# Kernel optimization log

Measured on AMD Instinct MI355X. Metric: run time of the kernel, lower is better.

## Reference

```python
import jax, jax.numpy as jnp
import numpy as np

H = 1024      # hidden_dim
V = 50257     # output_dim (vocab)
L = 512       # max_length


def setup_inputs() -> dict:
    key = jax.random.key(0)
    ks = jax.random.split(key, 12)
    s = 0.02
    return {
        "x": jax.random.randint(ks[0], (1,), 0, V),
        "hidden": jax.random.normal(ks[1], (1, 1, H), jnp.float32),
        "encoder_outputs": jax.random.normal(ks[2], (L, H), jnp.float32),
        "emb": jax.random.normal(ks[3], (V, H), jnp.float32) * s,
        "Ww": jax.random.normal(ks[4], (L, 2 * H), jnp.float32) * s,
        "bw": jnp.zeros((L,), jnp.float32),
        "Wc": jax.random.normal(ks[5], (H, 2 * H), jnp.float32) * s,
        "bc": jnp.zeros((H,), jnp.float32),
        "Wih": jax.random.normal(ks[6], (3 * H, H), jnp.float32) * s,
        "Whh": jax.random.normal(ks[7], (3 * H, H), jnp.float32) * s,
        "bih": jnp.zeros((3 * H,), jnp.float32),
        "bhh": jnp.zeros((3 * H,), jnp.float32),
        "Wo": jax.random.normal(ks[8], (V, H), jnp.float32) * s,
        "bo": jnp.zeros((V,), jnp.float32),
    }


def reference(x, hidden, encoder_outputs, emb, Ww, bw, Wc, bc, Wih, Whh, bih, bhh, Wo, bo):
    embed = emb[x].reshape(1, 1, -1)                      # [1,1,H]
    cat1 = jnp.concatenate([embed[0], hidden[0]], axis=1)  # [1,2H]
    weights = jax.nn.softmax(cat1 @ Ww.T + bw, axis=1)     # [1,L]
    wctx = weights @ encoder_outputs                       # [1,H]
    out = jnp.concatenate([embed[0], wctx], axis=1) @ Wc.T + bc  # [1,H]
    out = jax.nn.relu(out)
    # GRU cell (PyTorch gate layout: r, z, n)
    gi = out @ Wih.T + bih                                 # [1,3H]
    gh = hidden[0] @ Whh.T + bhh                           # [1,3H]
    r = jax.nn.sigmoid(gi[:, :H] + gh[:, :H])
    z = jax.nn.sigmoid(gi[:, H:2 * H] + gh[:, H:2 * H])
    n = jnp.tanh(gi[:, 2 * H:] + r * gh[:, 2 * H:])
    h_new = (1.0 - z) * n + z * hidden[0]                  # [1,H]
    logits = h_new @ Wo.T + bo                             # [1,V]
    out = jax.nn.log_softmax(logits, axis=1)
    return out, h_new[None], weights
```

## Files before the change

### kernel.cpp

```cpp
#include <hip/hip_runtime.h>
#include <math.h>

#define Hdim 1024
#define Vdim 50257
#define Ldim 512

__device__ __forceinline__ float waveReduceSum(float v) {
    #pragma unroll
    for (int off = 32; off > 0; off >>= 1) v += __shfl_down(v, off, 64);
    return v;
}
__device__ __forceinline__ float waveReduceMax(float v) {
    #pragma unroll
    for (int off = 32; off > 0; off >>= 1) v = fmaxf(v, __shfl_down(v, off, 64));
    return v;
}
template<int NW>
__device__ __forceinline__ float blockReduceSum(float v, float* red) {
    v = waveReduceSum(v);
    const int lane = threadIdx.x & 63, wid = threadIdx.x >> 6;
    if (lane == 0) red[wid] = v;
    __syncthreads();
    float s = red[0];
    #pragma unroll
    for (int i = 1; i < NW; i++) s += red[i];
    __syncthreads();
    return s;
}

__global__ __launch_bounds__(256) void k_att_gh(
    const int* __restrict__ xp, const float* __restrict__ hidden,
    const float* __restrict__ emb, const float* __restrict__ Ww,
    const float* __restrict__ bw, const float* __restrict__ Whh,
    const float* __restrict__ bhh, float* __restrict__ att, float* __restrict__ gh)
{
    __shared__ float red[4];
    const int t = threadIdx.x, bid = blockIdx.x;
    float acc = 0.f;
    if (bid < Ldim) {
        const int tok = xp[0];
        const float4* wrow = (const float4*)(Ww + (size_t)bid * (2 * Hdim));
        const float4* ev   = (const float4*)(emb + (size_t)tok * Hdim);
        const float4* hv   = (const float4*)hidden;
        #pragma unroll
        for (int k = 0; k < 2; ++k) {
            const int j = t * 2 + k;
            const float4 w = wrow[j];
            const float4 c = (j < Hdim / 4) ? ev[j] : hv[j - Hdim / 4];
            acc += w.x * c.x + w.y * c.y + w.z * c.z + w.w * c.w;
        }
        acc = blockReduceSum<4>(acc, red);
        if (t == 0) att[bid] = acc + bw[bid];
    } else {
        const int r = bid - Ldim;
        const float4* wrow = (const float4*)(Whh + (size_t)r * Hdim);
        const float4 w = wrow[t];
        const float4 h = ((const float4*)hidden)[t];
        acc = w.x * h.x + w.y * h.y + w.z * h.z + w.w * h.w;
        acc = blockReduceSum<4>(acc, red);
        if (t == 0) gh[r] = acc + bhh[r];
    }
}

__global__ __launch_bounds__(512) void k_softmax(
    const float* __restrict__ att, float* __restrict__ weights,
    float* __restrict__ out_w, float* __restrict__ wctx)
{
    __shared__ float red[8];
    __shared__ float bm, bs;
    const int t = threadIdx.x;
    const float v = att[t];
    float m = waveReduceMax(v);
    if ((t & 63) == 0) red[t >> 6] = m;
    __syncthreads();
    if (t == 0) {
        float mm = red[0];
        #pragma unroll
        for (int i = 1; i < 8; i++) mm = fmaxf(mm, red[i]);
        bm = mm;
    }
    __syncthreads();
    const float e = __expf(v - bm);
    float s = waveReduceSum(e);
    __syncthreads();
    if ((t & 63) == 0) red[t >> 6] = s;
    __syncthreads();
    if (t == 0) {
        float ss = red[0];
        #pragma unroll
        for (int i = 1; i < 8; i++) ss += red[i];
        bs = ss;
    }
    __syncthreads();
    const float w = e / bs;
    weights[t] = w;
    out_w[t]   = w;
    wctx[t] = 0.f; wctx[t + 512] = 0.f;
}

__global__ __launch_bounds__(256) void k_wctx(
    const float* __restrict__ weights, const float* __restrict__ enc,
    float* __restrict__ wctx)
{
    const int b = blockIdx.x, t = threadIdx.x;
    float4 acc = make_float4(0.f, 0.f, 0.f, 0.f);
    #pragma unroll
    for (int i = 0; i < 8; ++i) {
        const int l = b * 8 + i;
        const float w = weights[l];
        const float4 e = ((const float4*)(enc + (size_t)l * Hdim))[t];
        acc.x += w * e.x; acc.y += w * e.y; acc.z += w * e.z; acc.w += w * e.w;
    }
    atomicAdd(&wctx[t * 4 + 0], acc.x);
    atomicAdd(&wctx[t * 4 + 1], acc.y);
    atomicAdd(&wctx[t * 4 + 2], acc.z);
    atomicAdd(&wctx[t * 4 + 3], acc.w);
}

__global__ __launch_bounds__(256) void k_wc(
    const int* __restrict__ xp, const float* __restrict__ emb,
    const float* __restrict__ wctx, const float* __restrict__ Wc,
    const float* __restrict__ bc, float* __restrict__ cvec)
{
    __shared__ float red[4];
    const int t = threadIdx.x, r = blockIdx.x;
    const int tok = xp[0];
    const float4* wrow = (const float4*)(Wc + (size_t)r * (2 * Hdim));
    const float4* ev   = (const float4*)(emb + (size_t)tok * Hdim);
    const float4* cv   = (const float4*)wctx;
    float acc = 0.f;
    #pragma unroll
    for (int k = 0; k < 2; ++k) {
        const int j = t * 2 + k;
        const float4 w = wrow[j];
        const float4 c = (j < Hdim / 4) ? ev[j] : cv[j - Hdim / 4];
        acc += w.x * c.x + w.y * c.y + w.z * c.z + w.w * c.w;
    }
    acc = blockReduceSum<4>(acc, red);
    if (t == 0) cvec[r] = fmaxf(acc + bc[r], 0.f);
}

__global__ __launch_bounds__(256) void k_gru(
    const float* __restrict__ Wih, const float* __restrict__ bih,
    const float* __restrict__ gh, const float* __restrict__ cvec,
    const float* __restrict__ hidden, float* __restrict__ hnew,
    float* __restrict__ out_h)
{
    __shared__ float red[4];
    const int t = threadIdx.x, j = blockIdx.x;
    const float4 c = ((const float4*)cvec)[t];
    const float4 a = ((const float4*)(Wih + (size_t)j * Hdim))[t];
    const float4 b = ((const float4*)(Wih + (size_t)(j + Hdim) * Hdim))[t];
    const float4 d = ((const float4*)(Wih + (size_t)(j + 2 * Hdim) * Hdim))[t];
    float s0 = a.x * c.x + a.y * c.y + a.z * c.z + a.w * c.w;
    float s1 = b.x * c.x + b.y * c.y + b.z * c.z + b.w * c.w;
    float s2 = d.x * c.x + d.y * c.y + d.z * c.z + d.w * c.w;
    s0 = blockReduceSum<4>(s0, red);
    s1 = blockReduceSum<4>(s1, red);
    s2 = blockReduceSum<4>(s2, red);
    if (t == 0) {
        const float gir = s0 + bih[j];
        const float giz = s1 + bih[j + Hdim];
        const float gin = s2 + bih[j + 2 * Hdim];
        const float rr = 1.f / (1.f + __expf(-(gir + gh[j])));
        const float zz = 1.f / (1.f + __expf(-(giz + gh[j + Hdim])));
        const float nn = tanhf(gin + rr * gh[j + 2 * Hdim]);
        const float h = (1.f - zz) * nn + zz * hidden[j];
        hnew[j]  = h;
        out_h[j] = h;
    }
}

__global__ __launch_bounds__(256) void k_logits(
    const float* __restrict__ Wo, const float* __restrict__ bo,
    const float* __restrict__ h, float* __restrict__ logits)
{
    __shared__ float red[4];
    const int r = blockIdx.x, t = threadIdx.x;
    const float4 w = ((const float4*)(Wo + (size_t)r * Hdim))[t];
    const float4 hv = ((const float4*)h)[t];
    float acc = w.x * hv.x + w.y * hv.y + w.z * hv.z + w.w * hv.w;
    acc = waveReduceSum(acc);
    if ((t & 63) == 0) red[t >> 6] = acc;
    __syncthreads();
    if (t == 0) logits[r] = red[0] + red[1] + red[2] + red[3] + bo[r];
}

__global__ __launch_bounds__(256) void k_lse_part(
    const float* __restrict__ logits, float* __restrict__ pm, float* __restrict__ ps)
{
    __shared__ float redm[4], reds[4];
    const int gid = blockIdx.x * 256 + threadIdx.x;
    float m = -1e30f, s = 0.f;
    for (int i = gid; i < Vdim; i += 64 * 256) {
        const float v = logits[i];
        const float nm = fmaxf(m, v);
        s = s * __expf(m - nm) + __expf(v - nm);
        m = nm;
    }
    #pragma unroll
    for (int off = 32; off > 0; off >>= 1) {
        const float om = __shfl_down(m, off, 64);
        const float os = __shfl_down(s, off, 64);
        const float nm = fmaxf(m, om);
        s = s * __expf(m - nm) + os * __expf(om - nm);
        m = nm;
    }
    const int lane = threadIdx.x & 63, wid = threadIdx.x >> 6;
    if (lane == 0) { redm[wid] = m; reds[wid] = s; }
    __syncthreads();
    if (threadIdx.x == 0) {
        float M = redm[0], S = reds[0];
        #pragma unroll
        for (int i = 1; i < 4; i++) {
            const float nm = fmaxf(M, redm[i]);
            S = S * __expf(M - nm) + reds[i] * __expf(redm[i] - nm);
            M = nm;
        }
        pm[blockIdx.x] = M; ps[blockIdx.x] = S;
    }
}

__global__ __launch_bounds__(64) void k_lse_final(
    const float* __restrict__ pm, const float* __restrict__ ps,
    float* __restrict__ logZ)
{
    const int t = threadIdx.x;
    float m = pm[t], s = ps[t];
    #pragma unroll
    for (int off = 32; off > 0; off >>= 1) {
        const float om = __shfl_down(m, off, 64);
        const float os = __shfl_down(s, off, 64);
        const float nm = fmaxf(m, om);
        s = s * __expf(m - nm) + os * __expf(om - nm);
        m = nm;
    }
    if (t == 0) logZ[0] = m + logf(s);
}

__global__ __launch_bounds__(256) void k_out(
    float* __restrict__ out, const float* __restrict__ logZ)
{
    const int i = blockIdx.x * 256 + threadIdx.x;
    if (i < Vdim) out[i] = out[i] - logZ[0];
}

extern "C" void kernel_launch(void* const* d_in, const int* in_sizes, int n_in,
                              void* d_out, int out_size, void* d_ws, size_t ws_size,
                              hipStream_t stream)
{
    const int*   x      = (const int*)  d_in[0];
    const float* hidden = (const float*)d_in[1];
    const float* enc    = (const float*)d_in[2];
    const float* emb    = (const float*)d_in[3];
    const float* Ww     = (const float*)d_in[4];
    const float* bw     = (const float*)d_in[5];
    const float* Wc     = (const float*)d_in[6];
    const float* bc     = (const float*)d_in[7];
    const float* Wih    = (const float*)d_in[8];
    const float* Whh    = (const float*)d_in[9];
    const float* bih    = (const float*)d_in[10];
    const float* bhh    = (const float*)d_in[11];
    const float* Wo     = (const float*)d_in[12];
    const float* bo     = (const float*)d_in[13];

    float* out      = (float*)d_out;
    float* out_logp = out;
    float* out_h    = out + Vdim;
    float* out_w    = out + Vdim + Hdim;

    float* ws      = (float*)d_ws;
    float* att     = ws;
    float* weights = ws + 512;
    float* wctx    = ws + 1024;
    float* cvec    = ws + 2048;
    float* gh      = ws + 3072;
    float* hnew    = ws + 6144;
    float* pm      = ws + 7168;
    float* psum    = ws + 7232;
    float* logZ    = ws + 7296;

    k_att_gh   <<<dim3(Ldim + 3 * Hdim), dim3(256), 0, stream>>>(x, hidden, emb, Ww, bw, Whh, bhh, att, gh);
    k_softmax  <<<dim3(1),               dim3(512), 0, stream>>>(att, weights, out_w, wctx);
    k_wctx     <<<dim3(64),              dim3(256), 0, stream>>>(weights, enc, wctx);
    k_wc       <<<dim3(Hdim),            dim3(256), 0, stream>>>(x, emb, wctx, Wc, bc, cvec);
    k_gru      <<<dim3(Hdim),            dim3(256), 0, stream>>>(Wih, bih, gh, cvec, hidden, hnew, out_h);
    k_logits   <<<dim3(Vdim),            dim3(256), 0, stream>>>(Wo, bo, hnew, out_logp);
    k_lse_part <<<dim3(64),              dim3(256), 0, stream>>>(out_logp, pm, psum);
    k_lse_final<<<dim3(1),               dim3(64),  0, stream>>>(pm, psum, logZ);
    k_out      <<<dim3((Vdim + 255) / 256), dim3(256), 0, stream>>>(out_logp, logZ);
}
```

Measured before the change: 417.3 us.

## Fuse all decoder stages into one cooperative persistent kernel with grid syncs

Nine separate kernel launches become a single cooperative kernel of 256 blocks with 1024 threads each, using grid.sync between dependent phases. Each block redundantly computes the attention softmax into shared memory, replacing the separate softmax kernel and the atomic-based context accumulation. The logits GEMV now keeps one wave per row and folds the online log-sum-exp into the same pass, which removes the separate partial-reduction kernels. The aim is to cut launch overhead and extra passes over the logits. In exchange, each phase runs on a fixed 256-block grid with grid-wide barriers, and the 200MB Wo stream is read by fewer waves than before, which may lower memory-level parallelism.

```diff
diff --git a/kernel.cpp b/kernel.cpp
--- a/kernel.cpp
+++ b/kernel.cpp
@@ -1,9 +1,15 @@
 #include <hip/hip_runtime.h>
+#include <hip/hip_cooperative_groups.h>
 #include <math.h>
+
+namespace cg = cooperative_groups;
 
 #define Hdim 1024
 #define Vdim 50257
 #define Ldim 512
+#define NBLK 256
+#define NTHR 1024
+#define NWAVE 16
 
 __device__ __forceinline__ float waveReduceSum(float v) {
     #pragma unroll
@@ -15,234 +21,235 @@
     for (int off = 32; off > 0; off >>= 1) v = fmaxf(v, __shfl_down(v, off, 64));
     return v;
 }
-template<int NW>
-__device__ __forceinline__ float blockReduceSum(float v, float* red) {
-    v = waveReduceSum(v);
-    const int lane = threadIdx.x & 63, wid = threadIdx.x >> 6;
-    if (lane == 0) red[wid] = v;
-    __syncthreads();
-    float s = red[0];
-    #pragma unroll
-    for (int i = 1; i < NW; i++) s += red[i];
-    __syncthreads();
-    return s;
-}
-
-__global__ __launch_bounds__(256) void k_att_gh(
+__device__ __forceinline__ float dot4(float4 a, float4 b) {
+    return a.x * b.x + a.y * b.y + a.z * b.z + a.w * b.w;
+}
+
+__global__ __launch_bounds__(NTHR, 4) void k_fused(
     const int* __restrict__ xp, const float* __restrict__ hidden,
-    const float* __restrict__ emb, const float* __restrict__ Ww,
-    const float* __restrict__ bw, const float* __restrict__ Whh,
-    const float* __restrict__ bhh, float* __restrict__ att, float* __restrict__ gh)
+    const float* __restrict__ enc, const float* __restrict__ emb,
+    const float* __restrict__ Ww, const float* __restrict__ bw,
+    const float* __restrict__ Wc, const float* __restrict__ bc,
+    const float* __restrict__ Wih, const float* __restrict__ Whh,
+    const float* __restrict__ bih, const float* __restrict__ bhh,
+    const float* __restrict__ Wo, const float* __restrict__ bo,
+    float* __restrict__ out_logp, float* __restrict__ out_h,
+    float* __restrict__ out_w, float* __restrict__ ws)
 {
-    __shared__ float red[4];
-    const int t = threadIdx.x, bid = blockIdx.x;
-    float acc = 0.f;
-    if (bid < Ldim) {
-        const int tok = xp[0];
-        const float4* wrow = (const float4*)(Ww + (size_t)bid * (2 * Hdim));
-        const float4* ev   = (const float4*)(emb + (size_t)tok * Hdim);
-        const float4* hv   = (const float4*)hidden;
-        #pragma unroll
-        for (int k = 0; k < 2; ++k) {
-            const int j = t * 2 + k;
+    cg::grid_group grid = cg::this_grid();
+
+    __shared__ float sweights[Ldim];
+    __shared__ float red[NWAVE];
+    __shared__ float red2[NWAVE];
+    __shared__ float4 red4[8];
+    __shared__ float slz;
+
+    float* att  = ws;
+    float* gh   = ws + 512;
+    float* wctx = ws + 3584;
+    float* cvec = ws + 4608;
+    float* hnew = ws + 5632;
+    float* pm   = ws + 6656;
+    float* ps   = ws + 6912;
+
+    const int t = threadIdx.x, b = blockIdx.x;
+    const int lane = t & 63, iw = t >> 6;
+    const int tok = xp[0];
+    const float4* embv = (const float4*)(emb + (size_t)tok * Hdim);
+    const float4* hv   = (const float4*)hidden;
+
+    if (iw < 14) {
+        const int r = b * 14 + iw;
+        if (r < Ldim) {
+            const float4* wrow = (const float4*)(Ww + (size_t)r * (2 * Hdim));
+            float acc = 0.f;
+            #pragma unroll
+            for (int k = 0; k < 8; ++k) {
+                const int j = lane + 64 * k;
+                const float4 w = wrow[j];
+                const float4 c = (j < 256) ? embv[j] : hv[j - 256];
+                acc += dot4(w, c);
+            }
+            acc = waveReduceSum(acc);
+            if (lane == 0) att[r] = acc + bw[r];
+        } else {
+            const int r2 = r - Ldim;
+            const float4* wrow = (const float4*)(Whh + (size_t)r2 * Hdim);
+            float acc = 0.f;
+            #pragma unroll
+            for (int k = 0; k < 4; ++k) {
+                const int j = lane + 64 * k;
+                acc += dot4(wrow[j], hv[j]);
+            }
+            acc = waveReduceSum(acc);
+            if (lane == 0) gh[r2] = acc + bhh[r2];
+        }
+    }
+    grid.sync();
+
+    {
+        const float v = (t < Ldim) ? att[t] : -1e30f;
+        float wm = waveReduceMax(v);
+        if (lane == 0) red[iw] = wm;
+        __syncthreads();
+        float m = red[0];
+        #pragma unroll
+        for (int i = 1; i < NWAVE; ++i) m = fmaxf(m, red[i]);
+        const float e = (t < Ldim) ? __expf(v - m) : 0.f;
+        float wsum = waveReduceSum(e);
+        if (lane == 0) red2[iw] = wsum;
+        __syncthreads();
+        float s = red2[0];
+        #pragma unroll
+        for (int i = 1; i < NWAVE; ++i) s += red2[i];
+        if (t < Ldim) {
+            const float wgt = e / s;
+            sweights[t] = wgt;
+            if (b == 0) out_w[t] = wgt;
+        }
+    }
+
+    {
+        float4 acc = make_float4(0.f, 0.f, 0.f, 0.f);
+        if (t < Ldim) {
+            const float wgt = sweights[t];
+            const float4 e = *(const float4*)(enc + (size_t)t * Hdim + 4 * b);
+            acc.x = wgt * e.x; acc.y = wgt * e.y; acc.z = wgt * e.z; acc.w = wgt * e.w;
+        }
+        acc.x = waveReduceSum(acc.x);
+        acc.y = waveReduceSum(acc.y);
+        acc.z = waveReduceSum(acc.z);
+        acc.w = waveReduceSum(acc.w);
+        __syncthreads();
+        if (lane == 0 && iw < 8) red4[iw] = acc;
+        __syncthreads();
+        if (t == 0) {
+            float4 tot = red4[0];
+            #pragma unroll
+            for (int i = 1; i < 8; ++i) {
+                tot.x += red4[i].x; tot.y += red4[i].y;
+                tot.z += red4[i].z; tot.w += red4[i].w;
+            }
+            ((float4*)wctx)[b] = tot;
+        }
+    }
+    grid.sync();
+
+    if (iw < 4) {
+        const int r = b * 4 + iw;
+        const float4* wrow  = (const float4*)(Wc + (size_t)r * (2 * Hdim));
+        const float4* wctxv = (const float4*)wctx;
+        float acc = 0.f;
+        #pragma unroll
+        for (int k = 0; k < 8; ++k) {
+            const int j = lane + 64 * k;
             const float4 w = wrow[j];
-            const float4 c = (j < Hdim / 4) ? ev[j] : hv[j - Hdim / 4];
-            acc += w.x * c.x + w.y * c.y + w.z * c.z + w.w * c.w;
-        }
-        acc = blockReduceSum<4>(acc, red);
-        if (t == 0) att[bid] = acc + bw[bid];
-    } else {
-        const int r = bid - Ldim;
-        const float4* wrow = (const float4*)(Whh + (size_t)r * Hdim);
-        const float4 w = wrow[t];
-        const float4 h = ((const float4*)hidden)[t];
-        acc = w.x * h.x + w.y * h.y + w.z * h.z + w.w * h.w;
-        acc = blockReduceSum<4>(acc, red);
-        if (t == 0) gh[r] = acc + bhh[r];
-    }
-}
-
-__global__ __launch_bounds__(512) void k_softmax(
-    const float* __restrict__ att, float* __restrict__ weights,
-    float* __restrict__ out_w, float* __restrict__ wctx)
-{
-    __shared__ float red[8];
-    __shared__ float bm, bs;
-    const int t = threadIdx.x;
-    const float v = att[t];
-    float m = waveReduceMax(v);
-    if ((t & 63) == 0) red[t >> 6] = m;
-    __syncthreads();
-    if (t == 0) {
-        float mm = red[0];
-        #pragma unroll
-        for (int i = 1; i < 8; i++) mm = fmaxf(mm, red[i]);
-        bm = mm;
-    }
-    __syncthreads();
-    const float e = __expf(v - bm);
-    float s = waveReduceSum(e);
-    __syncthreads();
-    if ((t & 63) == 0) red[t >> 6] = s;
-    __syncthreads();
-    if (t == 0) {
-        float ss = red[0];
-        #pragma unroll
-        for (int i = 1; i < 8; i++) ss += red[i];
-        bs = ss;
-    }
-    __syncthreads();
-    const float w = e / bs;
-    weights[t] = w;
-    out_w[t]   = w;
-    wctx[t] = 0.f; wctx[t + 512] = 0.f;
-}
-
-__global__ __launch_bounds__(256) void k_wctx(
-    const float* __restrict__ weights, const float* __restrict__ enc,
-    float* __restrict__ wctx)
-{
-    const int b = blockIdx.x, t = threadIdx.x;
-    float4 acc = make_float4(0.f, 0.f, 0.f, 0.f);
-    #pragma unroll
-    for (int i = 0; i < 8; ++i) {
-        const int l = b * 8 + i;
-        const float w = weights[l];
-        const float4 e = ((const float4*)(enc + (size_t)l * Hdim))[t];
-        acc.x += w * e.x; acc.y += w * e.y; acc.z += w * e.z; acc.w += w * e.w;
-    }
-    atomicAdd(&wctx[t * 4 + 0], acc.x);
-    atomicAdd(&wctx[t * 4 + 1], acc.y);
-    atomicAdd(&wctx[t * 4 + 2], acc.z);
-    atomicAdd(&wctx[t * 4 + 3], acc.w);
-}
-
-__global__ __launch_bounds__(256) void k_wc(
-    const int* __restrict__ xp, const float* __restrict__ emb,
-    const float* __restrict__ wctx, const float* __restrict__ Wc,
-    const float* __restrict__ bc, float* __restrict__ cvec)
-{
-    __shared__ float red[4];
-    const int t = threadIdx.x, r = blockIdx.x;
-    const int tok = xp[0];
-    const float4* wrow = (const float4*)(Wc + (size_t)r * (2 * Hdim));
-    const float4* ev   = (const float4*)(emb + (size_t)tok * Hdim);
-    const float4* cv   = (const float4*)wctx;
-    float acc = 0.f;
-    #pragma unroll
-    for (int k = 0; k < 2; ++k) {
-        const int j = t * 2 + k;
-        const float4 w = wrow[j];
-        const float4 c = (j < Hdim / 4) ? ev[j] : cv[j - Hdim / 4];
-        acc += w.x * c.x + w.y * c.y + w.z * c.z + w.w * c.w;
-    }
-    acc = blockReduceSum<4>(acc, red);
-    if (t == 0) cvec[r] = fmaxf(acc + bc[r], 0.f);
-}
-
-__global__ __launch_bounds__(256) void k_gru(
-    const float* __restrict__ Wih, const float* __restrict__ bih,
-    const float* __restrict__ gh, const float* __restrict__ cvec,
-    const float* __restrict__ hidden, float* __restrict__ hnew,
-    float* __restrict__ out_h)
-{
-    __shared__ float red[4];
-    const int t = threadIdx.x, j = blockIdx.x;
-    const float4 c = ((const float4*)cvec)[t];
-    const float4 a = ((const float4*)(Wih + (size_t)j * Hdim))[t];
-    const float4 b = ((const float4*)(Wih + (size_t)(j + Hdim) * Hdim))[t];
-    const float4 d = ((const float4*)(Wih + (size_t)(j + 2 * Hdim) * Hdim))[t];
-    float s0 = a.x * c.x + a.y * c.y + a.z * c.z + a.w * c.w;
-    float s1 = b.x * c.x + b.y * c.y + b.z * c.z + b.w * c.w;
-    float s2 = d.x * c.x + d.y * c.y + d.z * c.z + d.w * c.w;
-    s0 = blockReduceSum<4>(s0, red);
-    s1 = blockReduceSum<4>(s1, red);
-    s2 = blockReduceSum<4>(s2, red);
-    if (t == 0) {
-        const float gir = s0 + bih[j];
-        const float giz = s1 + bih[j + Hdim];
-        const float gin = s2 + bih[j + 2 * Hdim];
-        const float rr = 1.f / (1.f + __expf(-(gir + gh[j])));
-        const float zz = 1.f / (1.f + __expf(-(giz + gh[j + Hdim])));
-        const float nn = tanhf(gin + rr * gh[j + 2 * Hdim]);
-        const float h = (1.f - zz) * nn + zz * hidden[j];
-        hnew[j]  = h;
-        out_h[j] = h;
-    }
-}
-
-__global__ __launch_bounds__(256) void k_logits(
-    const float* __restrict__ Wo, const float* __restrict__ bo,
-    const float* __restrict__ h, float* __restrict__ logits)
-{
-    __shared__ float red[4];
-    const int r = blockIdx.x, t = threadIdx.x;
-    const float4 w = ((const float4*)(Wo + (size_t)r * Hdim))[t];
-    const float4 hv = ((const float4*)h)[t];
-    float acc = w.x * hv.x + w.y * hv.y + w.z * hv.z + w.w * hv.w;
-    acc = waveReduceSum(acc);
-    if ((t & 63) == 0) red[t >> 6] = acc;
-    __syncthreads();
-    if (t == 0) logits[r] = red[0] + red[1] + red[2] + red[3] + bo[r];
-}
-
-__global__ __launch_bounds__(256) void k_lse_part(
-    const float* __restrict__ logits, float* __restrict__ pm, float* __restrict__ ps)
-{
-    __shared__ float redm[4], reds[4];
-    const int gid = blockIdx.x * 256 + threadIdx.x;
-    float m = -1e30f, s = 0.f;
-    for (int i = gid; i < Vdim; i += 64 * 256) {
-        const float v = logits[i];
-        const float nm = fmaxf(m, v);
-        s = s * __expf(m - nm) + __expf(v - nm);
-        m = nm;
-    }
-    #pragma unroll
-    for (int off = 32; off > 0; off >>= 1) {
-        const float om = __shfl_down(m, off, 64);
-        const float os = __shfl_down(s, off, 64);
-        const float nm = fmaxf(m, om);
-        s = s * __expf(m - nm) + os * __expf(om - nm);
-        m = nm;
-    }
-    const int lane = threadIdx.x & 63, wid = threadIdx.x >> 6;
-    if (lane == 0) { redm[wid] = m; reds[wid] = s; }
-    __syncthreads();
-    if (threadIdx.x == 0) {
-        float M = redm[0], S = reds[0];
-        #pragma unroll
-        for (int i = 1; i < 4; i++) {
-            const float nm = fmaxf(M, redm[i]);
-            S = S * __expf(M - nm) + reds[i] * __expf(redm[i] - nm);
-            M = nm;
-        }
-        pm[blockIdx.x] = M; ps[blockIdx.x] = S;
-    }
-}
-
-__global__ __launch_bounds__(64) void k_lse_final(
-    const float* __restrict__ pm, const float* __restrict__ ps,
-    float* __restrict__ logZ)
-{
-    const int t = threadIdx.x;
-    float m = pm[t], s = ps[t];
-    #pragma unroll
-    for (int off = 32; off > 0; off >>= 1) {
-        const float om = __shfl_down(m, off, 64);
-        const float os = __shfl_down(s, off, 64);
-        const float nm = fmaxf(m, om);
-        s = s * __expf(m - nm) + os * __expf(om - nm);
-        m = nm;
-    }
-    if (t == 0) logZ[0] = m + logf(s);
-}
-
-__global__ __launch_bounds__(256) void k_out(
-    float* __restrict__ out, const float* __restrict__ logZ)
-{
-    const int i = blockIdx.x * 256 + threadIdx.x;
-    if (i < Vdim) out[i] = out[i] - logZ[0];
+            const float4 c = (j < 256) ? embv[j] : wctxv[j - 256];
+            acc += dot4(w, c);
+        }
+        acc = waveReduceSum(acc);
+        if (lane == 0) cvec[r] = fmaxf(acc + bc[r], 0.f);
+    }
+    grid.sync();
+
+    if (iw < 4) {
+        const int j = b * 4 + iw;
+        const float4* cv = (const float4*)cvec;
+        const float4* a0 = (const float4*)(Wih + (size_t)j * Hdim);
+        const float4* a1 = (const float4*)(Wih + (size_t)(j + Hdim) * Hdim);
+        const float4* a2 = (const float4*)(Wih + (size_t)(j + 2 * Hdim) * Hdim);
+        float s0 = 0.f, s1 = 0.f, s2 = 0.f;
+        #pragma unroll
+        for (int k = 0; k < 4; ++k) {
+            const int jj = lane + 64 * k;
+            const float4 c = cv[jj];
+            s0 += dot4(a0[jj], c);
+            s1 += dot4(a1[jj], c);
+            s2 += dot4(a2[jj], c);
+        }
+        s0 = waveReduceSum(s0);
+        s1 = waveReduceSum(s1);
+        s2 = waveReduceSum(s2);
+        if (lane == 0) {
+            const float gir = s0 + bih[j];
+            const float giz = s1 + bih[j + Hdim];
+            const float gin = s2 + bih[j + 2 * Hdim];
+            const float rr = 1.f / (1.f + __expf(-(gir + gh[j])));
+            const float zz = 1.f / (1.f + __expf(-(giz + gh[j + Hdim])));
+            const float nn = tanhf(gin + rr * gh[j + 2 * Hdim]);
+            const float h = (1.f - zz) * nn + zz * hidden[j];
+            hnew[j]  = h;
+            out_h[j] = h;
+        }
+    }
+    grid.sync();
+
+    {
+        const float4* hv4 = (const float4*)hnew;
+        float4 hreg[4];
+        #pragma unroll
+        for (int k = 0; k < 4; ++k) hreg[k] = hv4[lane + 64 * k];
+
+        float m = -1e30f, s = 0.f;
+        const int g = b * NWAVE + iw;
+        for (int r = g; r < Vdim; r += NBLK * NWAVE) {
+            const float4* wrow = (const float4*)(Wo + (size_t)r * Hdim);
+            float acc = 0.f;
+            #pragma unroll
+            for (int k = 0; k < 4; ++k) acc += dot4(wrow[lane + 64 * k], hreg[k]);
+            acc = waveReduceSum(acc);
+            if (lane == 0) {
+                const float v = acc + bo[r];
+                out_logp[r] = v;
+                const float nm = fmaxf(m, v);
+                s = s * __expf(m - nm) + __expf(v - nm);
+                m = nm;
+            }
+        }
+        if (lane == 0) { red[iw] = m; red2[iw] = s; }
+        __syncthreads();
+        if (t == 0) {
+            float M = red[0], S = red2[0];
+            #pragma unroll
+            for (int i = 1; i < NWAVE; ++i) {
+                const float nm = fmaxf(M, red[i]);
+                S = S * __expf(M - nm) + red2[i] * __expf(red[i] - nm);
+                M = nm;
+            }
+            pm[b] = M; ps[b] = S;
+        }
+    }
+    grid.sync();
+
+    {
+        float m = -1e30f, s = 0.f;
+        if (t < NBLK) { m = pm[t]; s = ps[t]; }
+        #pragma unroll
+        for (int off = 32; off > 0; off >>= 1) {
+            const float om = __shfl_down(m, off, 64);
+            const float os = __shfl_down(s, off, 64);
+            const float nm = fmaxf(m, om);
+            s = s * __expf(m - nm) + os * __expf(om - nm);
+            m = nm;
+        }
+        __syncthreads();
+        if (lane == 0 && iw < 4) { red[iw] = m; red2[iw] = s; }
+        __syncthreads();
+        if (t == 0) {
+            float M = red[0], S = red2[0];
+            #pragma unroll
+            for (int i = 1; i < 4; ++i) {
+                const float nm = fmaxf(M, red[i]);
+                S = S * __expf(M - nm) + red2[i] * __expf(red[i] - nm);
+                M = nm;
+            }
+            slz = M + logf(S);
+        }
+        __syncthreads();
+        const float lz = slz;
+        const int i = b * NTHR + t;
+        if (i < Vdim) out_logp[i] -= lz;
+    }
 }
 
 extern "C" void kernel_launch(void* const* d_in, const int* in_sizes, int n_in,
@@ -268,25 +275,15 @@
     float* out_logp = out;
     float* out_h    = out + Vdim;
     float* out_w    = out + Vdim + Hdim;
-
-    float* ws      = (float*)d_ws;
-    float* att     = ws;
-    float* weights = ws + 512;
-    float* wctx    = ws + 1024;
-    float* cvec    = ws + 2048;
-    float* gh      = ws + 3072;
-    float* hnew    = ws + 6144;
-    float* pm      = ws + 7168;
-    float* psum    = ws + 7232;
-    float* logZ    = ws + 7296;
-
-    k_att_gh   <<<dim3(Ldim + 3 * Hdim), dim3(256), 0, stream>>>(x, hidden, emb, Ww, bw, Whh, bhh, att, gh);
-    k_softmax  <<<dim3(1),               dim3(512), 0, stream>>>(att, weights, out_w, wctx);
-    k_wctx     <<<dim3(64),              dim3(256), 0, stream>>>(weights, enc, wctx);
-    k_wc       <<<dim3(Hdim),            dim3(256), 0, stream>>>(x, emb, wctx, Wc, bc, cvec);
-    k_gru      <<<dim3(Hdim),            dim3(256), 0, stream>>>(Wih, bih, gh, cvec, hidden, hnew, out_h);
-    k_logits   <<<dim3(Vdim),            dim3(256), 0, stream>>>(Wo, bo, hnew, out_logp);
-    k_lse_part <<<dim3(64),              dim3(256), 0, stream>>>(out_logp, pm, psum);
-    k_lse_final<<<dim3(1),               dim3(64),  0, stream>>>(pm, psum, logZ);
-    k_out      <<<dim3((Vdim + 255) / 256), dim3(256), 0, stream>>>(out_logp, logZ);
-}
+    float* ws       = (float*)d_ws;
+
+    void* args[] = {
+        (void*)&x, (void*)&hidden, (void*)&enc, (void*)&emb,
+        (void*)&Ww, (void*)&bw, (void*)&Wc, (void*)&bc,
+        (void*)&Wih, (void*)&Whh, (void*)&bih, (void*)&bhh,
+        (void*)&Wo, (void*)&bo,
+        (void*)&out_logp, (void*)&out_h, (void*)&out_w, (void*)&ws
+    };
+    hipLaunchCooperativeKernel((const void*)k_fused, dim3(NBLK), dim3(NTHR),
+                               args, 0, stream);
+}
```

Measured after the change: 579.9 us. +39.0%, slower.

## Fuse softmax into wctx, wave-per-row logits with fused LSE partials

Applied to the files above, without the earlier changes.

Folds the attention softmax into every k_wctx block, which removes a single-block kernel launch, and moves the wctx zeroing into an extra block of k_att_gh. k_logits now gives one wavefront per vocab row (four rows per block) and has each block emit partial max/sum values. That removes the separate k_lse_part pass over the logits, and k_lse_final becomes a 1024-thread reduction over about 12.5K partials. Loads are coalesced by reading contiguous float4 halves, at the cost of redundant softmax work in each of the 64 wctx blocks.

```diff
diff --git a/kernel.cpp b/kernel.cpp
--- a/kernel.cpp
+++ b/kernel.cpp
@@ -4,6 +4,7 @@
 #define Hdim 1024
 #define Vdim 50257
 #define Ldim 512
+#define NB_LOG ((Vdim + 3) / 4)
 
 __device__ __forceinline__ float waveReduceSum(float v) {
     #pragma unroll
@@ -14,6 +15,9 @@
     #pragma unroll
     for (int off = 32; off > 0; off >>= 1) v = fmaxf(v, __shfl_down(v, off, 64));
     return v;
+}
+__device__ __forceinline__ float dot4(float4 a, float4 b) {
+    return a.x * b.x + a.y * b.y + a.z * b.z + a.w * b.w;
 }
 template<int NW>
 __device__ __forceinline__ float blockReduceSum(float v, float* red) {
@@ -32,82 +36,66 @@
     const int* __restrict__ xp, const float* __restrict__ hidden,
     const float* __restrict__ emb, const float* __restrict__ Ww,
     const float* __restrict__ bw, const float* __restrict__ Whh,
-    const float* __restrict__ bhh, float* __restrict__ att, float* __restrict__ gh)
+    const float* __restrict__ bhh, float* __restrict__ att,
+    float* __restrict__ gh, float* __restrict__ wctx)
 {
     __shared__ float red[4];
     const int t = threadIdx.x, bid = blockIdx.x;
+    if (bid == 3584) {
+        ((float4*)wctx)[t] = make_float4(0.f, 0.f, 0.f, 0.f);
+        return;
+    }
     float acc = 0.f;
     if (bid < Ldim) {
         const int tok = xp[0];
         const float4* wrow = (const float4*)(Ww + (size_t)bid * (2 * Hdim));
         const float4* ev   = (const float4*)(emb + (size_t)tok * Hdim);
         const float4* hv   = (const float4*)hidden;
-        #pragma unroll
-        for (int k = 0; k < 2; ++k) {
-            const int j = t * 2 + k;
-            const float4 w = wrow[j];
-            const float4 c = (j < Hdim / 4) ? ev[j] : hv[j - Hdim / 4];
-            acc += w.x * c.x + w.y * c.y + w.z * c.z + w.w * c.w;
-        }
+        const float4 w0 = wrow[t],        c0 = ev[t];
+        const float4 w1 = wrow[t + 256],  c1 = hv[t];
+        acc = dot4(w0, c0) + dot4(w1, c1);
         acc = blockReduceSum<4>(acc, red);
         if (t == 0) att[bid] = acc + bw[bid];
     } else {
         const int r = bid - Ldim;
         const float4* wrow = (const float4*)(Whh + (size_t)r * Hdim);
-        const float4 w = wrow[t];
-        const float4 h = ((const float4*)hidden)[t];
-        acc = w.x * h.x + w.y * h.y + w.z * h.z + w.w * h.w;
+        acc = dot4(wrow[t], ((const float4*)hidden)[t]);
         acc = blockReduceSum<4>(acc, red);
         if (t == 0) gh[r] = acc + bhh[r];
     }
 }
 
-__global__ __launch_bounds__(512) void k_softmax(
-    const float* __restrict__ att, float* __restrict__ weights,
-    float* __restrict__ out_w, float* __restrict__ wctx)
-{
-    __shared__ float red[8];
+__global__ __launch_bounds__(256) void k_wctx(
+    const float* __restrict__ att, const float* __restrict__ enc,
+    float* __restrict__ wctx, float* __restrict__ out_w)
+{
+    __shared__ float red[4];
+    __shared__ float sw[Ldim];
     __shared__ float bm, bs;
-    const int t = threadIdx.x;
-    const float v = att[t];
-    float m = waveReduceMax(v);
-    if ((t & 63) == 0) red[t >> 6] = m;
-    __syncthreads();
-    if (t == 0) {
-        float mm = red[0];
-        #pragma unroll
-        for (int i = 1; i < 8; i++) mm = fmaxf(mm, red[i]);
-        bm = mm;
-    }
-    __syncthreads();
-    const float e = __expf(v - bm);
-    float s = waveReduceSum(e);
-    __syncthreads();
-    if ((t & 63) == 0) red[t >> 6] = s;
-    __syncthreads();
-    if (t == 0) {
-        float ss = red[0];
-        #pragma unroll
-        for (int i = 1; i < 8; i++) ss += red[i];
-        bs = ss;
-    }
-    __syncthreads();
-    const float w = e / bs;
-    weights[t] = w;
-    out_w[t]   = w;
-    wctx[t] = 0.f; wctx[t + 512] = 0.f;
-}
-
-__global__ __launch_bounds__(256) void k_wctx(
-    const float* __restrict__ weights, const float* __restrict__ enc,
-    float* __restrict__ wctx)
-{
-    const int b = blockIdx.x, t = threadIdx.x;
+    const int t = threadIdx.x, lane = t & 63, iw = t >> 6;
+    const float v0 = att[t], v1 = att[t + 256];
+    float m = waveReduceMax(fmaxf(v0, v1));
+    if (lane == 0) red[iw] = m;
+    __syncthreads();
+    if (t == 0) bm = fmaxf(fmaxf(red[0], red[1]), fmaxf(red[2], red[3]));
+    __syncthreads();
+    const float e0 = __expf(v0 - bm), e1 = __expf(v1 - bm);
+    float s = waveReduceSum(e0 + e1);
+    __syncthreads();
+    if (lane == 0) red[iw] = s;
+    __syncthreads();
+    if (t == 0) bs = red[0] + red[1] + red[2] + red[3];
+    __syncthreads();
+    const float w0 = e0 / bs, w1 = e1 / bs;
+    sw[t] = w0; sw[t + 256] = w1;
+    if (blockIdx.x == 0) { out_w[t] = w0; out_w[t + 256] = w1; }
+    __syncthreads();
+
     float4 acc = make_float4(0.f, 0.f, 0.f, 0.f);
     #pragma unroll
     for (int i = 0; i < 8; ++i) {
-        const int l = b * 8 + i;
-        const float w = weights[l];
+        const int l = blockIdx.x * 8 + i;
+        const float w = sw[l];
         const float4 e = ((const float4*)(enc + (size_t)l * Hdim))[t];
         acc.x += w * e.x; acc.y += w * e.y; acc.z += w * e.z; acc.w += w * e.w;
     }
@@ -128,14 +116,7 @@
     const float4* wrow = (const float4*)(Wc + (size_t)r * (2 * Hdim));
     const float4* ev   = (const float4*)(emb + (size_t)tok * Hdim);
     const float4* cv   = (const float4*)wctx;
-    float acc = 0.f;
-    #pragma unroll
-    for (int k = 0; k < 2; ++k) {
-        const int j = t * 2 + k;
-        const float4 w = wrow[j];
-        const float4 c = (j < Hdim / 4) ? ev[j] : cv[j - Hdim / 4];
-        acc += w.x * c.x + w.y * c.y + w.z * c.z + w.w * c.w;
-    }
+    float acc = dot4(wrow[t], ev[t]) + dot4(wrow[t + 256], cv[t]);
     acc = blockReduceSum<4>(acc, red);
     if (t == 0) cvec[r] = fmaxf(acc + bc[r], 0.f);
 }
@@ -152,9 +133,7 @@
     const float4 a = ((const float4*)(Wih + (size_t)j * Hdim))[t];
     const float4 b = ((const float4*)(Wih + (size_t)(j + Hdim) * Hdim))[t];
     const float4 d = ((const float4*)(Wih + (size_t)(j + 2 * Hdim) * Hdim))[t];
-    float s0 = a.x * c.x + a.y * c.y + a.z * c.z + a.w * c.w;
-    float s1 = b.x * c.x + b.y * c.y + b.z * c.z + b.w * c.w;
-    float s2 = d.x * c.x + d.y * c.y + d.z * c.z + d.w * c.w;
+    float s0 = dot4(a, c), s1 = dot4(b, c), s2 = dot4(d, c);
     s0 = blockReduceSum<4>(s0, red);
     s1 = blockReduceSum<4>(s1, red);
     s2 = blockReduceSum<4>(s2, red);
@@ -173,29 +152,48 @@
 
 __global__ __launch_bounds__(256) void k_logits(
     const float* __restrict__ Wo, const float* __restrict__ bo,
-    const float* __restrict__ h, float* __restrict__ logits)
-{
-    __shared__ float red[4];
-    const int r = blockIdx.x, t = threadIdx.x;
-    const float4 w = ((const float4*)(Wo + (size_t)r * Hdim))[t];
-    const float4 hv = ((const float4*)h)[t];
-    float acc = w.x * hv.x + w.y * hv.y + w.z * hv.z + w.w * hv.w;
-    acc = waveReduceSum(acc);
-    if ((t & 63) == 0) red[t >> 6] = acc;
-    __syncthreads();
-    if (t == 0) logits[r] = red[0] + red[1] + red[2] + red[3] + bo[r];
-}
-
-__global__ __launch_bounds__(256) void k_lse_part(
-    const float* __restrict__ logits, float* __restrict__ pm, float* __restrict__ ps)
-{
-    __shared__ float redm[4], reds[4];
-    const int gid = blockIdx.x * 256 + threadIdx.x;
-    float m = -1e30f, s = 0.f;
-    for (int i = gid; i < Vdim; i += 64 * 256) {
-        const float v = logits[i];
-        const float nm = fmaxf(m, v);
-        s = s * __expf(m - nm) + __expf(v - nm);
+    const float* __restrict__ h, float* __restrict__ logits,
+    float* __restrict__ pm, float* __restrict__ ps)
+{
+    __shared__ float redv[4];
+    const int t = threadIdx.x, lane = t & 63, iw = t >> 6;
+    const int r = blockIdx.x * 4 + iw;
+    float v = -INFINITY;
+    if (r < Vdim) {
+        const float4* wrow = (const float4*)(Wo + (size_t)r * Hdim);
+        const float4* hv   = (const float4*)h;
+        float acc = 0.f;
+        #pragma unroll
+        for (int k = 0; k < 4; ++k)
+            acc += dot4(wrow[lane + 64 * k], hv[lane + 64 * k]);
+        acc = waveReduceSum(acc);
+        if (lane == 0) {
+            v = acc + bo[r];
+            logits[r] = v;
+        }
+    }
+    if (lane == 0) redv[iw] = v;
+    __syncthreads();
+    if (t == 0) {
+        float m = fmaxf(fmaxf(redv[0], redv[1]), fmaxf(redv[2], redv[3]));
+        float s = 0.f;
+        #pragma unroll
+        for (int i = 0; i < 4; ++i) s += __expf(redv[i] - m);
+        pm[blockIdx.x] = m; ps[blockIdx.x] = s;
+    }
+}
+
+__global__ __launch_bounds__(1024) void k_lse_final(
+    const float* __restrict__ pm, const float* __restrict__ ps,
+    float* __restrict__ logZ)
+{
+    __shared__ float redm[16], reds[16];
+    const int t = threadIdx.x, lane = t & 63, iw = t >> 6;
+    float m = -INFINITY, s = 0.f;
+    for (int i = t; i < NB_LOG; i += 1024) {
+        const float om = pm[i], os = ps[i];
+        const float nm = fmaxf(m, om);
+        s = s * __expf(m - nm) + os * __expf(om - nm);
         m = nm;
     }
     #pragma unroll
@@ -206,36 +204,18 @@
         s = s * __expf(m - nm) + os * __expf(om - nm);
         m = nm;
     }
-    const int lane = threadIdx.x & 63, wid = threadIdx.x >> 6;
-    if (lane == 0) { redm[wid] = m; reds[wid] = s; }
-    __syncthreads();
-    if (threadIdx.x == 0) {
+    if (lane == 0) { redm[iw] = m; reds[iw] = s; }
+    __syncthreads();
+    if (t == 0) {
         float M = redm[0], S = reds[0];
         #pragma unroll
-        for (int i = 1; i < 4; i++) {
+        for (int i = 1; i < 16; ++i) {
             const float nm = fmaxf(M, redm[i]);
             S = S * __expf(M - nm) + reds[i] * __expf(redm[i] - nm);
             M = nm;
         }
-        pm[blockIdx.x] = M; ps[blockIdx.x] = S;
-    }
-}
-
-__global__ __launch_bounds__(64) void k_lse_final(
-    const float* __restrict__ pm, const float* __restrict__ ps,
-    float* __restrict__ logZ)
-{
-    const int t = threadIdx.x;
-    float m = pm[t], s = ps[t];
-    #pragma unroll
-    for (int off = 32; off > 0; off >>= 1) {
-        const float om = __shfl_down(m, off, 64);
-        const float os = __shfl_down(s, off, 64);
-        const float nm = fmaxf(m, om);
-        s = s * __expf(m - nm) + os * __expf(om - nm);
-        m = nm;
-    }
-    if (t == 0) logZ[0] = m + logf(s);
+        logZ[0] = M + logf(S);
+    }
 }
 
 __global__ __launch_bounds__(256) void k_out(
@@ -269,24 +249,21 @@
     float* out_h    = out + Vdim;
     float* out_w    = out + Vdim + Hdim;
 
-    float* ws      = (float*)d_ws;
-    float* att     = ws;
-    float* weights = ws + 512;
-    float* wctx    = ws + 1024;
-    float* cvec    = ws + 2048;
-    float* gh      = ws + 3072;
-    float* hnew    = ws + 6144;
-    float* pm      = ws + 7168;
-    float* psum    = ws + 7232;
-    float* logZ    = ws + 7296;
-
-    k_att_gh   <<<dim3(Ldim + 3 * Hdim), dim3(256), 0, stream>>>(x, hidden, emb, Ww, bw, Whh, bhh, att, gh);
-    k_softmax  <<<dim3(1),               dim3(512), 0, stream>>>(att, weights, out_w, wctx);
-    k_wctx     <<<dim3(64),              dim3(256), 0, stream>>>(weights, enc, wctx);
-    k_wc       <<<dim3(Hdim),            dim3(256), 0, stream>>>(x, emb, wctx, Wc, bc, cvec);
-    k_gru      <<<dim3(Hdim),            dim3(256), 0, stream>>>(Wih, bih, gh, cvec, hidden, hnew, out_h);
-    k_logits   <<<dim3(Vdim),            dim3(256), 0, stream>>>(Wo, bo, hnew, out_logp);
-    k_lse_part <<<dim3(64),              dim3(256), 0, stream>>>(out_logp, pm, psum);
-    k_lse_final<<<dim3(1),               dim3(64),  0, stream>>>(pm, psum, logZ);
+    float* ws   = (float*)d_ws;
+    float* att  = ws;
+    float* gh   = ws + 512;
+    float* wctx = ws + 3584;
+    float* cvec = ws + 4608;
+    float* hnew = ws + 5632;
+    float* pm   = ws + 6656;
+    float* psum = ws + 6656 + NB_LOG;
+    float* logZ = ws + 6656 + 2 * NB_LOG;
+
+    k_att_gh   <<<dim3(3585),             dim3(256),  0, stream>>>(x, hidden, emb, Ww, bw, Whh, bhh, att, gh, wctx);
+    k_wctx     <<<dim3(64),               dim3(256),  0, stream>>>(att, enc, wctx, out_w);
+    k_wc       <<<dim3(Hdim),             dim3(256),  0, stream>>>(x, emb, wctx, Wc, bc, cvec);
+    k_gru      <<<dim3(Hdim),             dim3(256),  0, stream>>>(Wih, bih, gh, cvec, hidden, hnew, out_h);
+    k_logits   <<<dim3(NB_LOG),           dim3(256),  0, stream>>>(Wo, bo, hnew, out_logp, pm, psum);
+    k_lse_final<<<dim3(1),                dim3(1024), 0, stream>>>(pm, psum, logZ);
     k_out      <<<dim3((Vdim + 255) / 256), dim3(256), 0, stream>>>(out_logp, logZ);
 }
```

Measured after the change: 423.9 us. No clear change (+1.6%).
